# Performance work log

Hardware: AMD Instinct MI355X
Metric: run time of the kernel (lower is better)

Reference implementation:

```python
import jax, jax.numpy as jnp
import numpy as np

EMB = 1024
HEADS = 16

def setup_inputs() -> dict:
    key = jax.random.key(0)
    ks = jax.random.split(key, 5)
    s = 1.0 / np.sqrt(EMB)
    x = jax.random.normal(ks[0], (2, 2048, EMB), dtype=jnp.float32)
    W_qkv = jax.random.normal(ks[1], (EMB, 3 * EMB), dtype=jnp.float32) * s
    b_qkv = jnp.zeros((3 * EMB,), dtype=jnp.float32)
    W_out = jax.random.normal(ks[2], (EMB, EMB), dtype=jnp.float32) * s
    b_out = jnp.zeros((EMB,), dtype=jnp.float32)
    return {"x": x, "W_qkv": W_qkv, "b_qkv": b_qkv, "W_out": W_out, "b_out": b_out}

def reference(x, W_qkv, b_qkv, W_out, b_out):
    B, N, C = x.shape
    H = HEADS
    D = C // H
    qkv = x @ W_qkv + b_qkv                      # [B,N,3C]
    qkv = qkv.reshape(B, N, 3, H, D)
    q, k, v = (qkv[:, :, i].transpose(0, 2, 1, 3) for i in range(3))  # [B,H,N,D]
    # NOTE: original scales by C**-0.5 (full embed dim), not head dim
    scale = C ** (-0.5)
    attn = jnp.einsum('bhnd,bhmd->bhnm', q, k) * scale
    attn = jax.nn.softmax(attn, axis=-1)
    out = jnp.einsum('bhnm,bhmd->bhnd', attn, v)  # [B,H,N,D]
    out = out.transpose(0, 2, 1, 3).reshape(B, N, C)
    return out @ W_out + b_out
```

## Files before the change

### kernel.cpp

```cpp
#include <hip/hip_runtime.h>
#include <hip/hip_bf16.h>
#include <cstdint>
#include <cstddef>

typedef __bf16 bf16;
typedef __bf16 bf16x4 __attribute__((ext_vector_type(4)));
typedef __bf16 bf16x8 __attribute__((ext_vector_type(8)));
typedef float f32x4 __attribute__((ext_vector_type(4)));

#define LOG2E 1.4426950408889634f
#define QSCALE (0.03125f * LOG2E)
#define PSHIFT 8.0f

#define GLD16(gp, lp)                                                              \
  __builtin_amdgcn_global_load_lds((__attribute__((address_space(1))) void*)(gp),  \
                                   (__attribute__((address_space(3))) void*)(lp),  \
                                   16, 0, 0)

__global__ void k_prep(const float* __restrict__ x, const float* __restrict__ Wqkv,
                       const float* __restrict__ Wout, bf16* __restrict__ xb,
                       bf16* __restrict__ wqT, bf16* __restrict__ woT) {
  const int blk = blockIdx.x, tid = threadIdx.x;
  if (blk < 2048) {
    int i = (blk * 256 + tid) * 8;
    const float4* p = (const float4*)(x + i);
    float4 a = p[0], b = p[1];
    bf16x8 o;
    o[0] = (bf16)a.x; o[1] = (bf16)a.y; o[2] = (bf16)a.z; o[3] = (bf16)a.w;
    o[4] = (bf16)b.x; o[5] = (bf16)b.y; o[6] = (bf16)b.z; o[7] = (bf16)b.w;
    *(bf16x8*)(xb + i) = o;
    return;
  }
  const float* in;
  bf16* out;
  int R = 1024, C, bx, by;
  if (blk < 2048 + 3072) {
    in = Wqkv; out = wqT; C = 3072;
    bx = (blk - 2048) % 96; by = (blk - 2048) / 96;
  } else {
    in = Wout; out = woT; C = 1024;
    bx = (blk - 5120) % 32; by = (blk - 5120) / 32;
  }
  __shared__ float t[32][33];
  const int tx = tid & 31, ty = tid >> 5;
  int c0 = bx * 32, r0 = by * 32;
#pragma unroll
  for (int i = 0; i < 4; i++)
    t[ty + i * 8][tx] = in[(size_t)(r0 + ty + i * 8) * C + c0 + tx];
  __syncthreads();
#pragma unroll
  for (int i = 0; i < 4; i++)
    out[(size_t)(c0 + ty + i * 8) * R + r0 + tx] = (bf16)t[tx][ty + i * 8];
}

template <int EPI>
__global__ __launch_bounds__(256, 2) void k_gemm_bt(
    const bf16* __restrict__ A, const bf16* __restrict__ Bt,
    const float* __restrict__ bias, float* __restrict__ outF,
    bf16* __restrict__ qb, bf16* __restrict__ kb, bf16* __restrict__ vb) {
  __shared__ __align__(16) bf16 As[128 * 32];
  __shared__ __align__(16) bf16 Bs[128 * 32];
  const int tid = threadIdx.x;
  const int lane = tid & 63, w = tid >> 6;
  const int quad = lane >> 4, l16 = lane & 15;
  const int wm = (w >> 1) * 64, wn = (w & 1) * 64;
  const int bm = blockIdx.y * 128, bn = blockIdx.x * 128;
  f32x4 acc[4][4] = {};

  for (int kt = 0; kt < 1024; kt += 32) {
    __syncthreads();
#pragma unroll
    for (int p = 0; p < 2; p++) {
      int idx = p * 256 + tid;
      int row = idx >> 2, bq = idx & 3;
      int gb = (bq - ((row >> 1) & 3)) & 3;
      GLD16(A + (size_t)(bm + row) * 1024 + kt + gb * 8, As + idx * 8);
      GLD16(Bt + (size_t)(bn + row) * 1024 + kt + gb * 8, Bs + idx * 8);
    }
    __syncthreads();

    bf16x8 af[4], bfr[4];
#pragma unroll
    for (int mi = 0; mi < 4; mi++) {
      int row = wm + mi * 16 + l16;
      int bq = (quad + ((row >> 1) & 3)) & 3;
      af[mi] = *(const bf16x8*)(As + row * 32 + bq * 8);
    }
#pragma unroll
    for (int ni = 0; ni < 4; ni++) {
      int row = wn + ni * 16 + l16;
      int bq = (quad + ((row >> 1) & 3)) & 3;
      bfr[ni] = *(const bf16x8*)(Bs + row * 32 + bq * 8);
    }
#pragma unroll
    for (int mi = 0; mi < 4; mi++)
#pragma unroll
      for (int ni = 0; ni < 4; ni++)
        acc[mi][ni] =
            __builtin_amdgcn_mfma_f32_16x16x32_bf16(af[mi], bfr[ni], acc[mi][ni], 0, 0, 0);
  }

#pragma unroll
  for (int ni = 0; ni < 4; ni++) {
    int col = bn + wn + ni * 16 + l16;
    float bv = bias[col];
    if (EPI == 1) {
#pragma unroll
      for (int mi = 0; mi < 4; mi++)
#pragma unroll
        for (int r = 0; r < 4; r++) {
          int row = bm + wm + mi * 16 + quad * 4 + r;
          outF[(size_t)row * 1024 + col] = acc[mi][ni][r] + bv;
        }
    } else {
      int which = col >> 10, cc = col & 1023;
      int h = cc >> 6, d = cc & 63;
      if (which == 2) {
#pragma unroll
        for (int mi = 0; mi < 4; mi++) {
          int rowb = bm + wm + mi * 16 + quad * 4;
          int b = rowb >> 11, n0 = rowb & 2047;
          bf16x4 vv;
#pragma unroll
          for (int r = 0; r < 4; r++) vv[r] = (bf16)(acc[mi][ni][r] + bv);
          *(bf16x4*)(vb + ((size_t)(b * 16 + h) * 64 + d) * 2048 + n0) = vv;
        }
      } else {
#pragma unroll
        for (int mi = 0; mi < 4; mi++)
#pragma unroll
          for (int r = 0; r < 4; r++) {
            int row = bm + wm + mi * 16 + quad * 4 + r;
            int b = row >> 11, n = row & 2047;
            float v = acc[mi][ni][r] + bv;
            if (which == 0)
              qb[((size_t)(b * 16 + h) * 2048 + n) * 64 + d] = (bf16)(v * QSCALE);
            else
              kb[((size_t)(b * 16 + h) * 2048 + n) * 64 + d] = (bf16)v;
          }
      }
    }
  }
}

__global__ __launch_bounds__(256, 4) void k_flash(
    const bf16* __restrict__ Q, const bf16* __restrict__ K,
    const bf16* __restrict__ V, bf16* __restrict__ O) {
  __shared__ __align__(16) bf16 Kt[2][64 * 64];
  __shared__ __align__(16) bf16 Vt[2][64 * 64];
  __shared__ __align__(16) bf16 Pb[4][16 * 64];
  const int tid = threadIdx.x;
  const int lane = tid & 63, w = tid >> 6;
  const int quad = lane >> 4, l16 = lane & 15;
  const int bh = blockIdx.y, qt = blockIdx.x;
  const bf16* qh = Q + (size_t)bh * 2048 * 64;
  const bf16* kh = K + (size_t)bh * 2048 * 64;
  const bf16* vh = V + (size_t)bh * 64 * 2048;

  bf16x8 qf[2];
#pragma unroll
  for (int kc = 0; kc < 2; kc++)
    qf[kc] = *(const bf16x8*)(qh + (size_t)(qt * 64 + w * 16 + l16) * 64 + kc * 32 + quad * 8);

  bf16x8 ones;
#pragma unroll
  for (int j = 0; j < 8; j++) ones[j] = (bf16)1.0f;

  f32x4 o[4] = {};
  f32x4 lacc = {};

  bf16* pw = &Pb[w][0];

  auto stage = [&](int kt2, int buf) {
#pragma unroll
    for (int p = 0; p < 2; p++) {
      int idx = p * 256 + tid;
      int row = idx >> 3, bq = idx & 7, gb = bq ^ (row & 7);
      GLD16(kh + (size_t)(kt2 * 64 + row) * 64 + gb * 8, &Kt[buf][idx * 8]);
      GLD16(vh + (size_t)row * 2048 + kt2 * 64 + gb * 8, &Vt[buf][idx * 8]);
    }
  };

  stage(0, 0);

  for (int kt2 = 0; kt2 < 32; kt2++) {
    const int p = kt2 & 1;
    __syncthreads();
    if (kt2 < 31) stage(kt2 + 1, p ^ 1);
    const bf16* Kb = &Kt[p][0];
    const bf16* Vb = &Vt[p][0];

    f32x4 s[4];
#pragma unroll
    for (int nj = 0; nj < 4; nj++) {
      int row = nj * 16 + l16;
      bf16x8 kf0 = *(const bf16x8*)(Kb + row * 64 + ((quad ^ (row & 7)) << 3));
      bf16x8 kf1 = *(const bf16x8*)(Kb + row * 64 + (((4 + quad) ^ (row & 7)) << 3));
      f32x4 t = {-PSHIFT, -PSHIFT, -PSHIFT, -PSHIFT};
      t = __builtin_amdgcn_mfma_f32_16x16x32_bf16(kf0, qf[0], t, 0, 0, 0);
      t = __builtin_amdgcn_mfma_f32_16x16x32_bf16(kf1, qf[1], t, 0, 0, 0);
      s[nj] = t;
    }

    {
      bf16* pr = pw + l16 * 64;
#pragma unroll
      for (int nj = 0; nj < 4; nj++) {
        bf16x4 pk;
#pragma unroll
        for (int r = 0; r < 4; r++) pk[r] = (bf16)__builtin_amdgcn_exp2f(s[nj][r]);
        int blk = (nj * 2 + (quad >> 1)) ^ (l16 & 7);
        *(bf16x4*)(pr + blk * 8 + (quad & 1) * 4) = pk;
      }
    }

#pragma unroll
    for (int kc = 0; kc < 2; kc++) {
      bf16x8 pf =
          *(const bf16x8*)(pw + l16 * 64 + (((kc * 4 + quad) ^ (l16 & 7)) << 3));
      lacc = __builtin_amdgcn_mfma_f32_16x16x32_bf16(ones, pf, lacc, 0, 0, 0);
#pragma unroll
      for (int nd = 0; nd < 4; nd++) {
        int row = nd * 16 + l16;
        bf16x8 vf = *(const bf16x8*)(Vb + row * 64 + (((kc * 4 + quad) ^ (row & 7)) << 3));
        o[nd] = __builtin_amdgcn_mfma_f32_16x16x32_bf16(vf, pf, o[nd], 0, 0, 0);
      }
    }
  }

  const int b = bh >> 4, h = bh & 15;
  float inv = 1.0f / lacc[0];
  int n = qt * 64 + w * 16 + l16;
#pragma unroll
  for (int nd = 0; nd < 4; nd++) {
    bf16x4 ov;
#pragma unroll
    for (int r = 0; r < 4; r++) ov[r] = (bf16)(o[nd][r] * inv);
    int c = h * 64 + nd * 16 + quad * 4;
    *(bf16x4*)(O + ((size_t)b * 2048 + n) * 1024 + c) = ov;
  }
}


extern "C" void kernel_launch(void* const* d_in, const int* in_sizes, int n_in,
                              void* d_out, int out_size, void* d_ws, size_t ws_size,
                              hipStream_t stream) {
  (void)in_sizes; (void)n_in; (void)out_size; (void)ws_size;
  const float* x    = (const float*)d_in[0];
  const float* Wqkv = (const float*)d_in[1];
  const float* bqkv = (const float*)d_in[2];
  const float* Wout = (const float*)d_in[3];
  const float* bout = (const float*)d_in[4];
  float* out = (float*)d_out;

  char* ws = (char*)d_ws;
  size_t off = 0;
  auto take = [&](size_t bytes) {
    char* p = ws + off;
    off += (bytes + 255) & ~(size_t)255;
    return p;
  };
  bf16* xb   = (bf16*)take((size_t)4096 * 1024 * 2);
  bf16* wqT  = (bf16*)take((size_t)3072 * 1024 * 2);
  bf16* woT  = (bf16*)take((size_t)1024 * 1024 * 2);
  bf16* qbuf = (bf16*)take((size_t)32 * 2048 * 64 * 2);
  bf16* kbuf = (bf16*)take((size_t)32 * 2048 * 64 * 2);
  bf16* vbuf = (bf16*)take((size_t)32 * 2048 * 64 * 2);
  bf16* aout = (bf16*)take((size_t)4096 * 1024 * 2);

  k_prep<<<6144, 256, 0, stream>>>(x, Wqkv, Wout, xb, wqT, woT);
  k_gemm_bt<0><<<dim3(24, 32), 256, 0, stream>>>(xb, wqT, bqkv, nullptr, qbuf, kbuf, vbuf);
  k_flash<<<dim3(32, 32), 256, 0, stream>>>(qbuf, kbuf, vbuf, aout);
  k_gemm_bt<1><<<dim3(8, 32), 256, 0, stream>>>(aout, woT, bout, out, nullptr, nullptr, nullptr);
}
```

Before: 190.6 us.

## Double GEMM K-tile and restructure flash attention into 2x2 wave tiling

The QKV/out GEMM now stages 64-wide K slices with XOR swizzling instead of 32-wide ones, halving the barrier count per output tile. The flash kernel splits the four waves into a 2x2 grid over query rows and key/head-dim columns. Each wave computes a 32x32 score block, so K and V fragments are reused across two query tiles. P is shared through padded LDS between wave pairs with an extra barrier, and the row sums are accumulated in registers and combined via LDS instead of a ones-vector MFMA. Occupancy hint drops from 4 to 3 blocks and LDS use grows.

```diff
diff --git a/kernel.cpp b/kernel.cpp
--- a/kernel.cpp
+++ b/kernel.cpp
@@ -58,8 +58,8 @@
     const bf16* __restrict__ A, const bf16* __restrict__ Bt,
     const float* __restrict__ bias, float* __restrict__ outF,
     bf16* __restrict__ qb, bf16* __restrict__ kb, bf16* __restrict__ vb) {
-  __shared__ __align__(16) bf16 As[128 * 32];
-  __shared__ __align__(16) bf16 Bs[128 * 32];
+  __shared__ __align__(16) bf16 As[128 * 64];
+  __shared__ __align__(16) bf16 Bs[128 * 64];
   const int tid = threadIdx.x;
   const int lane = tid & 63, w = tid >> 6;
   const int quad = lane >> 4, l16 = lane & 15;
@@ -67,37 +67,38 @@
   const int bm = blockIdx.y * 128, bn = blockIdx.x * 128;
   f32x4 acc[4][4] = {};
 
-  for (int kt = 0; kt < 1024; kt += 32) {
-    __syncthreads();
-#pragma unroll
-    for (int p = 0; p < 2; p++) {
+  for (int kt = 0; kt < 1024; kt += 64) {
+    __syncthreads();
+#pragma unroll
+    for (int p = 0; p < 4; p++) {
       int idx = p * 256 + tid;
-      int row = idx >> 2, bq = idx & 3;
-      int gb = (bq - ((row >> 1) & 3)) & 3;
+      int row = idx >> 3, bq = idx & 7;
+      int gb = bq ^ (row & 7);
       GLD16(A + (size_t)(bm + row) * 1024 + kt + gb * 8, As + idx * 8);
       GLD16(Bt + (size_t)(bn + row) * 1024 + kt + gb * 8, Bs + idx * 8);
     }
     __syncthreads();
 
-    bf16x8 af[4], bfr[4];
-#pragma unroll
-    for (int mi = 0; mi < 4; mi++) {
-      int row = wm + mi * 16 + l16;
-      int bq = (quad + ((row >> 1) & 3)) & 3;
-      af[mi] = *(const bf16x8*)(As + row * 32 + bq * 8);
-    }
-#pragma unroll
-    for (int ni = 0; ni < 4; ni++) {
-      int row = wn + ni * 16 + l16;
-      int bq = (quad + ((row >> 1) & 3)) & 3;
-      bfr[ni] = *(const bf16x8*)(Bs + row * 32 + bq * 8);
-    }
-#pragma unroll
-    for (int mi = 0; mi < 4; mi++)
-#pragma unroll
-      for (int ni = 0; ni < 4; ni++)
-        acc[mi][ni] =
-            __builtin_amdgcn_mfma_f32_16x16x32_bf16(af[mi], bfr[ni], acc[mi][ni], 0, 0, 0);
+#pragma unroll
+    for (int s = 0; s < 2; s++) {
+      bf16x8 af[4], bfr[4];
+#pragma unroll
+      for (int mi = 0; mi < 4; mi++) {
+        int row = wm + mi * 16 + l16;
+        af[mi] = *(const bf16x8*)(As + row * 64 + (((s * 4 + quad) ^ (row & 7)) << 3));
+      }
+#pragma unroll
+      for (int ni = 0; ni < 4; ni++) {
+        int row = wn + ni * 16 + l16;
+        bfr[ni] = *(const bf16x8*)(Bs + row * 64 + (((s * 4 + quad) ^ (row & 7)) << 3));
+      }
+#pragma unroll
+      for (int mi = 0; mi < 4; mi++)
+#pragma unroll
+        for (int ni = 0; ni < 4; ni++)
+          acc[mi][ni] =
+              __builtin_amdgcn_mfma_f32_16x16x32_bf16(af[mi], bfr[ni], acc[mi][ni], 0, 0, 0);
+    }
   }
 
 #pragma unroll
@@ -143,101 +144,124 @@
   }
 }
 
-__global__ __launch_bounds__(256, 4) void k_flash(
+__global__ __launch_bounds__(256, 3) void k_flash(
     const bf16* __restrict__ Q, const bf16* __restrict__ K,
     const bf16* __restrict__ V, bf16* __restrict__ O) {
   __shared__ __align__(16) bf16 Kt[2][64 * 64];
   __shared__ __align__(16) bf16 Vt[2][64 * 64];
-  __shared__ __align__(16) bf16 Pb[4][16 * 64];
+  __shared__ __align__(16) bf16 Ps[2][32 * 72];
+  __shared__ float Ls[64][2];
   const int tid = threadIdx.x;
   const int lane = tid & 63, w = tid >> 6;
   const int quad = lane >> 4, l16 = lane & 15;
-  const int bh = blockIdx.y, qt = blockIdx.x;
+  const int kw = w & 1, qw = w >> 1;
+  const int bh = blockIdx.y, qb = blockIdx.x;
   const bf16* qh = Q + (size_t)bh * 2048 * 64;
   const bf16* kh = K + (size_t)bh * 2048 * 64;
   const bf16* vh = V + (size_t)bh * 64 * 2048;
 
-  bf16x8 qf[2];
-#pragma unroll
-  for (int kc = 0; kc < 2; kc++)
-    qf[kc] = *(const bf16x8*)(qh + (size_t)(qt * 64 + w * 16 + l16) * 64 + kc * 32 + quad * 8);
-
-  bf16x8 ones;
-#pragma unroll
-  for (int j = 0; j < 8; j++) ones[j] = (bf16)1.0f;
-
-  f32x4 o[4] = {};
-  f32x4 lacc = {};
-
-  bf16* pw = &Pb[w][0];
-
-  auto stage = [&](int kt2, int buf) {
+  bf16x8 qf[2][2];
+#pragma unroll
+  for (int qt = 0; qt < 2; qt++)
+#pragma unroll
+    for (int kc = 0; kc < 2; kc++)
+      qf[qt][kc] = *(const bf16x8*)(qh + (size_t)(qb * 64 + qw * 32 + qt * 16 + l16) * 64 +
+                                    kc * 32 + quad * 8);
+
+  f32x4 o[2][2] = {};
+  float lp[2] = {0.f, 0.f};
+
+  bf16* ps = &Ps[qw][0];
+
+  auto stage = [&](int kt, int buf) {
 #pragma unroll
     for (int p = 0; p < 2; p++) {
       int idx = p * 256 + tid;
       int row = idx >> 3, bq = idx & 7, gb = bq ^ (row & 7);
-      GLD16(kh + (size_t)(kt2 * 64 + row) * 64 + gb * 8, &Kt[buf][idx * 8]);
-      GLD16(vh + (size_t)row * 2048 + kt2 * 64 + gb * 8, &Vt[buf][idx * 8]);
+      GLD16(kh + (size_t)(kt * 64 + row) * 64 + gb * 8, &Kt[buf][idx * 8]);
+      GLD16(vh + (size_t)row * 2048 + kt * 64 + gb * 8, &Vt[buf][idx * 8]);
     }
   };
 
   stage(0, 0);
 
-  for (int kt2 = 0; kt2 < 32; kt2++) {
-    const int p = kt2 & 1;
-    __syncthreads();
-    if (kt2 < 31) stage(kt2 + 1, p ^ 1);
+  for (int kt = 0; kt < 32; kt++) {
+    const int p = kt & 1;
+    __syncthreads();
+    if (kt < 31) stage(kt + 1, p ^ 1);
     const bf16* Kb = &Kt[p][0];
     const bf16* Vb = &Vt[p][0];
 
-    f32x4 s[4];
-#pragma unroll
-    for (int nj = 0; nj < 4; nj++) {
-      int row = nj * 16 + l16;
-      bf16x8 kf0 = *(const bf16x8*)(Kb + row * 64 + ((quad ^ (row & 7)) << 3));
-      bf16x8 kf1 = *(const bf16x8*)(Kb + row * 64 + (((4 + quad) ^ (row & 7)) << 3));
-      f32x4 t = {-PSHIFT, -PSHIFT, -PSHIFT, -PSHIFT};
-      t = __builtin_amdgcn_mfma_f32_16x16x32_bf16(kf0, qf[0], t, 0, 0, 0);
-      t = __builtin_amdgcn_mfma_f32_16x16x32_bf16(kf1, qf[1], t, 0, 0, 0);
-      s[nj] = t;
-    }
-
-    {
-      bf16* pr = pw + l16 * 64;
-#pragma unroll
-      for (int nj = 0; nj < 4; nj++) {
-        bf16x4 pk;
-#pragma unroll
-        for (int r = 0; r < 4; r++) pk[r] = (bf16)__builtin_amdgcn_exp2f(s[nj][r]);
-        int blk = (nj * 2 + (quad >> 1)) ^ (l16 & 7);
-        *(bf16x4*)(pr + blk * 8 + (quad & 1) * 4) = pk;
-      }
-    }
+    f32x4 s[2][2];
+#pragma unroll
+    for (int knj = 0; knj < 2; knj++) {
+      int krow = kw * 32 + knj * 16 + l16;
+      bf16x8 kf0 = *(const bf16x8*)(Kb + krow * 64 + ((quad ^ (krow & 7)) << 3));
+      bf16x8 kf1 = *(const bf16x8*)(Kb + krow * 64 + (((4 + quad) ^ (krow & 7)) << 3));
+#pragma unroll
+      for (int qt = 0; qt < 2; qt++) {
+        f32x4 t = {-PSHIFT, -PSHIFT, -PSHIFT, -PSHIFT};
+        t = __builtin_amdgcn_mfma_f32_16x16x32_bf16(kf0, qf[qt][0], t, 0, 0, 0);
+        t = __builtin_amdgcn_mfma_f32_16x16x32_bf16(kf1, qf[qt][1], t, 0, 0, 0);
+        s[knj][qt] = t;
+      }
+    }
+
+#pragma unroll
+    for (int knj = 0; knj < 2; knj++)
+#pragma unroll
+      for (int qt = 0; qt < 2; qt++) {
+        float p0 = __builtin_amdgcn_exp2f(s[knj][qt][0]);
+        float p1 = __builtin_amdgcn_exp2f(s[knj][qt][1]);
+        float p2 = __builtin_amdgcn_exp2f(s[knj][qt][2]);
+        float p3 = __builtin_amdgcn_exp2f(s[knj][qt][3]);
+        lp[qt] += (p0 + p1) + (p2 + p3);
+        bf16x4 pk = {(bf16)p0, (bf16)p1, (bf16)p2, (bf16)p3};
+        *(bf16x4*)(ps + (qt * 16 + l16) * 72 + kw * 32 + knj * 16 + quad * 4) = pk;
+      }
+
+    __syncthreads();
 
 #pragma unroll
     for (int kc = 0; kc < 2; kc++) {
-      bf16x8 pf =
-          *(const bf16x8*)(pw + l16 * 64 + (((kc * 4 + quad) ^ (l16 & 7)) << 3));
-      lacc = __builtin_amdgcn_mfma_f32_16x16x32_bf16(ones, pf, lacc, 0, 0, 0);
-#pragma unroll
-      for (int nd = 0; nd < 4; nd++) {
-        int row = nd * 16 + l16;
-        bf16x8 vf = *(const bf16x8*)(Vb + row * 64 + (((kc * 4 + quad) ^ (row & 7)) << 3));
-        o[nd] = __builtin_amdgcn_mfma_f32_16x16x32_bf16(vf, pf, o[nd], 0, 0, 0);
-      }
-    }
-  }
-
+      bf16x8 pf[2];
+#pragma unroll
+      for (int qt = 0; qt < 2; qt++)
+        pf[qt] = *(const bf16x8*)(ps + (qt * 16 + l16) * 72 + kc * 32 + quad * 8);
+#pragma unroll
+      for (int dnj = 0; dnj < 2; dnj++) {
+        int drow = kw * 32 + dnj * 16 + l16;
+        bf16x8 vf = *(const bf16x8*)(Vb + drow * 64 + (((kc * 4 + quad) ^ (drow & 7)) << 3));
+        o[dnj][0] = __builtin_amdgcn_mfma_f32_16x16x32_bf16(vf, pf[0], o[dnj][0], 0, 0, 0);
+        o[dnj][1] = __builtin_amdgcn_mfma_f32_16x16x32_bf16(vf, pf[1], o[dnj][1], 0, 0, 0);
+      }
+    }
+  }
+
+#pragma unroll
+  for (int qt = 0; qt < 2; qt++) {
+    lp[qt] += __shfl_xor(lp[qt], 16, 64);
+    lp[qt] += __shfl_xor(lp[qt], 32, 64);
+  }
+  if (lane < 16) {
+    Ls[qw * 32 + lane][kw] = lp[0];
+    Ls[qw * 32 + 16 + lane][kw] = lp[1];
+  }
+  __syncthreads();
   const int b = bh >> 4, h = bh & 15;
-  float inv = 1.0f / lacc[0];
-  int n = qt * 64 + w * 16 + l16;
-#pragma unroll
-  for (int nd = 0; nd < 4; nd++) {
-    bf16x4 ov;
-#pragma unroll
-    for (int r = 0; r < 4; r++) ov[r] = (bf16)(o[nd][r] * inv);
-    int c = h * 64 + nd * 16 + quad * 4;
-    *(bf16x4*)(O + ((size_t)b * 2048 + n) * 1024 + c) = ov;
+#pragma unroll
+  for (int qt = 0; qt < 2; qt++) {
+    int q = qw * 32 + qt * 16 + l16;
+    float inv = 1.0f / (Ls[q][0] + Ls[q][1]);
+    int n = qb * 64 + q;
+#pragma unroll
+    for (int dnj = 0; dnj < 2; dnj++) {
+      bf16x4 ov;
+#pragma unroll
+      for (int r = 0; r < 4; r++) ov[r] = (bf16)(o[dnj][qt][r] * inv);
+      int c = h * 64 + kw * 32 + dnj * 16 + quad * 4;
+      *(bf16x4*)(O + ((size_t)b * 2048 + n) * 1024 + c) = ov;
+    }
   }
 }
 
```

Result: slower. 213.5 us (+12.0%).
